# Kernel tuning notes

Hardware: AMD Instinct MI355X
Metric: run time of the kernel (lower is better)

The kernel has to match this reference:

```python
import jax, jax.numpy as jnp
import numpy as np

N = 100000   # nodes
E = 1600000  # edges


def setup_inputs() -> dict:
    key = jax.random.key(0)
    ks = jax.random.split(key, 9)
    return {
        "in_feat": jax.random.normal(ks[0], (N, 256), jnp.float32),
        "W": jax.random.normal(ks[1], (256, 128), jnp.float32) * 0.05,
        "attn_l": jax.random.normal(ks[2], (1, 128), jnp.float32) * 0.1,
        "attn_r": jax.random.normal(ks[3], (1, 128), jnp.float32) * 0.1,
        "bias": jax.random.normal(ks[4], (1, 128), jnp.float32) * 0.01,
        "fc_w": jax.random.normal(ks[5], (128, 2), jnp.float32) * 0.1,
        "fc_b": jax.random.normal(ks[6], (2,), jnp.float32) * 0.01,
        "src": jax.random.randint(ks[7], (E,), 0, N, jnp.int32),
        "dst": jax.random.randint(ks[8], (E,), 0, N, jnp.int32),
    }


def reference(in_feat, W, attn_l, attn_r, bias, fc_w, fc_b, src, dst):
    # GATConv, num_heads=1 (head dim kept implicit since it is squeezed anyway)
    h = in_feat @ W                              # [N, F] projected features
    el = jnp.sum(h * attn_l, axis=-1)            # [N] left attention logits
    er = jnp.sum(h * attn_r, axis=-1)            # [N] right attention logits
    e = jax.nn.leaky_relu(el[src] + er[dst], negative_slope=0.2)  # [E]
    # edge softmax segmented by destination node (numerically stable)
    m = jax.ops.segment_max(e, dst, num_segments=N)               # [N]
    ex = jnp.exp(e - m[dst])                                      # [E]
    s = jax.ops.segment_sum(ex, dst, num_segments=N)              # [N]
    alpha = ex / jnp.where(s == 0, 1.0, s)[dst]                   # [E]
    # attention-weighted aggregation of source features to destinations
    agg = jax.ops.segment_sum(alpha[:, None] * h[src], dst, num_segments=N)  # [N, F]
    agg = agg + bias                                              # GATConv bias
    # head: ReLU -> Linear -> sigmoid
    out = jax.nn.sigmoid(jax.nn.relu(agg) @ fc_w + fc_b)          # [N, C]
    return out
```

## Files before the change

### kernel.cpp

```cpp
#include <hip/hip_runtime.h>
#include <cstdint>
#include <cstddef>

#define N_NODES 100000
#define E_EDGES 1600000
#define F_IN 256
#define F_OUT 128
#define NBKT 391
#define OBCAP 5120

#define GLOBAL_AS __attribute__((address_space(1)))
#define LDS_AS    __attribute__((address_space(3)))

typedef __attribute__((ext_vector_type(8))) short  short8v;
typedef __attribute__((ext_vector_type(4))) float  float4v;

__device__ __forceinline__ unsigned short f2bf(float x) {
    union { float f; unsigned u; } v; v.f = x;
    unsigned r = v.u + 0x7fffu + ((v.u >> 16) & 1u);
    return (unsigned short)(r >> 16);
}

__device__ __forceinline__ unsigned cvt_pk_bf16(float lo, float hi) {
    unsigned r;
    asm("v_cvt_pk_bf16_f32 %0, %1, %2" : "=v"(r) : "v"(lo), "v"(hi));
    return r;
}

__global__ __launch_bounds__(256) void wcvt_kernel(const float* __restrict__ W,
                                                   unsigned short* __restrict__ Wt) {
    int t = blockIdx.x * 256 + threadIdx.x;
    if (t >= F_IN * F_OUT) return;
    int k = t >> 7, j = t & 127;
    Wt[j * F_IN + k] = f2bf(W[t]);
}

__global__ __launch_bounds__(256) void gemm_mfma(const float* __restrict__ A,
                                                 const unsigned short* __restrict__ Wt,
                                                 const float* __restrict__ attn_l,
                                                 const float* __restrict__ attn_r,
                                                 unsigned short* __restrict__ Hb,
                                                 float* __restrict__ el,
                                                 float* __restrict__ er) {
    __shared__ float          Afs[64 * 64];
    __shared__ unsigned short Bs[128 * 64];
    int tid  = threadIdx.x;
    int wave = tid >> 6, lane = tid & 63;
    int g = lane >> 4, c = lane & 15;
    int row0 = blockIdx.x * 64;
    float4v acc[8] = {};

    int a_r[4], a_k[4], a_w[4];
    #pragma unroll
    for (int i = 0; i < 4; ++i) {
        int W_ = i * 1024 + tid * 4;
        int r  = W_ >> 6;
        a_w[i] = W_;
        a_r[i] = min(row0 + r, N_NODES - 1);
        a_k[i] = (W_ & 63) ^ ((r & 15) << 2);
    }
    int b_j[4], b_k[4], b_u[4];
    #pragma unroll
    for (int i = 0; i < 4; ++i) {
        int U_ = i * 2048 + tid * 8;
        int j  = U_ >> 6;
        b_u[i] = U_;
        b_j[i] = j;
        b_k[i] = (U_ & 63) ^ ((j & 7) << 3);
    }

    for (int k0 = 0; k0 < F_IN; k0 += 64) {
        #pragma unroll
        for (int i = 0; i < 4; ++i) {
            __builtin_amdgcn_global_load_lds(
                (const GLOBAL_AS unsigned int*)(A + (size_t)a_r[i] * F_IN + k0 + a_k[i]),
                (LDS_AS unsigned int*)&Afs[a_w[i]], 16, 0, 0);
        }
        #pragma unroll
        for (int i = 0; i < 4; ++i) {
            __builtin_amdgcn_global_load_lds(
                (const GLOBAL_AS unsigned int*)(Wt + (size_t)b_j[i] * F_IN + k0 + b_k[i]),
                (LDS_AS unsigned int*)&Bs[b_u[i]], 16, 0, 0);
        }
        __syncthreads();
        int arow = wave * 16 + c;
        int aswz = (arow & 15) << 2;
        #pragma unroll
        for (int ks = 0; ks < 2; ++ks) {
            int woff = arow * 64 + ks * 32 + g * 8;
            float4 a0 = *reinterpret_cast<float4*>(&Afs[(woff)     ^ aswz]);
            float4 a1 = *reinterpret_cast<float4*>(&Afs[(woff + 4) ^ aswz]);
            unsigned u[4];
            u[0] = cvt_pk_bf16(a0.x, a0.y);
            u[1] = cvt_pk_bf16(a0.z, a0.w);
            u[2] = cvt_pk_bf16(a1.x, a1.y);
            u[3] = cvt_pk_bf16(a1.z, a1.w);
            short8v af = *reinterpret_cast<short8v*>(u);
            #pragma unroll
            for (int nt = 0; nt < 8; ++nt) {
                int j = nt * 16 + c;
                int boff = (j * 64 + ks * 32 + g * 8) ^ ((j & 7) << 3);
                short8v bf = *reinterpret_cast<short8v*>(&Bs[boff]);
                acc[nt] = __builtin_amdgcn_mfma_f32_16x16x32_bf16(af, bf, acc[nt], 0, 0, 0);
            }
        }
        __syncthreads();
    }

    float al[8], ar[8];
    #pragma unroll
    for (int nt = 0; nt < 8; ++nt) {
        al[nt] = attn_l[nt * 16 + c];
        ar[nt] = attn_r[nt * 16 + c];
    }
    #pragma unroll
    for (int r = 0; r < 4; ++r) {
        int grow = row0 + wave * 16 + g * 4 + r;
        float sl = 0.f, sr = 0.f;
        #pragma unroll
        for (int nt = 0; nt < 8; ++nt) {
            float h = acc[nt][r];
            sl += h * al[nt];
            sr += h * ar[nt];
        }
        if (grow < N_NODES) {
            #pragma unroll
            for (int nt = 0; nt < 8; ++nt)
                Hb[(size_t)grow * F_OUT + nt * 16 + c] = f2bf(acc[nt][r]);
        }
        #pragma unroll
        for (int off = 1; off < 16; off <<= 1) {
            sl += __shfl_xor(sl, off);
            sr += __shfl_xor(sr, off);
        }
        if (c == 0 && grow < N_NODES) { el[grow] = sl; er[grow] = sr; }
    }
}

__global__ __launch_bounds__(256) void k_hist1(const int* __restrict__ dst,
                                               int* __restrict__ bcnt) {
    __shared__ int h[NBKT];
    int t = threadIdx.x;
    for (int i = t; i < NBKT; i += 256) h[i] = 0;
    __syncthreads();
    int e0  = blockIdx.x * 4096;
    int end = min(e0 + 4096, E_EDGES);
    for (int i = e0 + t; i < end; i += 256) atomicAdd(&h[dst[i] >> 8], 1);
    __syncthreads();
    for (int i = t; i < NBKT; i += 256) if (h[i]) atomicAdd(&bcnt[i], h[i]);
}

__global__ __launch_bounds__(512) void k_scan(const int* __restrict__ bcnt,
                                              int* __restrict__ bbase,
                                              int* __restrict__ bcur) {
    __shared__ int s[512];
    int t = threadIdx.x;
    int d = (t < NBKT) ? bcnt[t] : 0;
    s[t] = d;
    __syncthreads();
    for (int off = 1; off < 512; off <<= 1) {
        int v = (t >= off) ? s[t - off] : 0;
        __syncthreads();
        s[t] += v;
        __syncthreads();
    }
    if (t < NBKT) { int ex = s[t] - d; bbase[t] = ex; bcur[t] = ex; }
    if (t == NBKT - 1) bbase[NBKT] = s[t];
}

__global__ __launch_bounds__(256) void k_scatter1(const int* __restrict__ src,
                                                  const int* __restrict__ dst,
                                                  int* __restrict__ bcur,
                                                  unsigned int* __restrict__ epack) {
    __shared__ int h[NBKT];
    int t = threadIdx.x;
    for (int i = t; i < NBKT; i += 256) h[i] = 0;
    __syncthreads();
    int e0  = blockIdx.x * 4096;
    int end = min(e0 + 4096, E_EDGES);
    #pragma unroll
    for (int j = 0; j < 16; ++j) {
        int i = e0 + j * 256 + t;
        if (i < end) atomicAdd(&h[dst[i] >> 8], 1);
    }
    __syncthreads();
    for (int i = t; i < NBKT; i += 256) {
        int c = h[i];
        h[i] = c ? atomicAdd(&bcur[i], c) : 0;
    }
    __syncthreads();
    #pragma unroll
    for (int j = 0; j < 16; ++j) {
        int i = e0 + j * 256 + t;
        if (i < end) {
            int dv = dst[i];
            int p = atomicAdd(&h[dv >> 8], 1);
            epack[p] = (unsigned)src[i] | ((unsigned)(dv & 255) << 17);
        }
    }
}

__global__ __launch_bounds__(256) void k_sort2(const unsigned int* __restrict__ epack,
                                               const int* __restrict__ bbase,
                                               int* __restrict__ esrc,
                                               int* __restrict__ rowptr,
                                               int* __restrict__ deg) {
    __shared__ int hist[256], cur[256], s[256];
    __shared__ int obuf[OBCAP];
    int b = blockIdx.x, t = threadIdx.x;
    int base = bbase[b], end = bbase[b + 1];
    int cnt  = end - base;
    hist[t] = 0;
    __syncthreads();
    for (int i = t; i < cnt; i += 256) atomicAdd(&hist[epack[base + i] >> 17], 1);
    __syncthreads();
    int d = hist[t];
    s[t] = d;
    __syncthreads();
    for (int off = 1; off < 256; off <<= 1) {
        int v = (t >= off) ? s[t - off] : 0;
        __syncthreads();
        s[t] += v;
        __syncthreads();
    }
    int excl = s[t] - d;
    int n = b * 256 + t;
    if (n < N_NODES) { deg[n] = d; rowptr[n] = base + excl; }
    cur[t] = excl;
    __syncthreads();
    for (int i = t; i < cnt; i += 256) {
        unsigned e = epack[base + i];
        int p = atomicAdd(&cur[e >> 17], 1);
        if (p < OBCAP) obuf[p] = (int)(e & 0x1FFFFu);
    }
    __syncthreads();
    for (int i = t; i < cnt; i += 256) esrc[base + i] = obuf[i];
}

__global__ __launch_bounds__(256) void agg_fused(const int* __restrict__ rowptr,
                                                 const int* __restrict__ deg,
                                                 const int* __restrict__ esrc,
                                                 const float* __restrict__ el,
                                                 const float* __restrict__ er,
                                                 const char* __restrict__ Hc,
                                                 const float* __restrict__ bias,
                                                 const float* __restrict__ fcw,
                                                 const float* __restrict__ fcb,
                                                 float* __restrict__ out) {
    __shared__ float2 exbuf[4][64];
    int tid   = threadIdx.x;
    int wslot = tid >> 6;
    int wid   = (blockIdx.x * 256 + tid) >> 6;
    int lane  = tid & 63;
    if (wid >= N_NODES) return;
    int grp = lane >> 4, fl = lane & 15;
    int start = rowptr[wid];
    int dg    = deg[wid];
    float ern = er[wid];
    float exsum = 0.f;
    float acc[8] = {};
    float2* eb = exbuf[wslot];
    unsigned flb = (unsigned)fl << 4;

    for (int base = 0; base < dg; base += 64) {
        int cnt = min(64, dg - base);
        unsigned rowb = 0;
        float ex = 0.f;
        if (lane < cnt) {
            int sid = esrc[start + base + lane];
            float tv = el[(unsigned)sid] + ern;
            tv = tv > 0.f ? tv : 0.2f * tv;
            ex = __expf(tv);
            rowb = (unsigned)sid << 8;
        }
        exsum += ex;
        eb[lane] = make_float2(ex, __uint_as_float(rowb));
        __builtin_amdgcn_wave_barrier();
        int nq = (cnt + 3) >> 2;
        #pragma unroll 2
        for (int q = 0; q < nq; ++q) {
            float2 p = eb[q * 4 + grp];
            float exq = p.x;
            uint4 v = *(const uint4*)(Hc + (__float_as_uint(p.y) + flb));
            acc[0] += exq * __uint_as_float(v.x << 16);
            acc[1] += exq * __uint_as_float(v.x & 0xffff0000u);
            acc[2] += exq * __uint_as_float(v.y << 16);
            acc[3] += exq * __uint_as_float(v.y & 0xffff0000u);
            acc[4] += exq * __uint_as_float(v.z << 16);
            acc[5] += exq * __uint_as_float(v.z & 0xffff0000u);
            acc[6] += exq * __uint_as_float(v.w << 16);
            acc[7] += exq * __uint_as_float(v.w & 0xffff0000u);
        }
        __builtin_amdgcn_wave_barrier();
    }

    #pragma unroll
    for (int j = 0; j < 8; ++j) {
        acc[j] += __shfl_xor(acc[j], 16);
        acc[j] += __shfl_xor(acc[j], 32);
    }
    float ssum = exsum;
    #pragma unroll
    for (int off = 32; off; off >>= 1) ssum += __shfl_xor(ssum, off);
    float scale = ssum > 0.f ? 1.f / ssum : 0.f;

    float4 b0 = ((const float4*)bias)[fl * 2];
    float4 b1 = ((const float4*)bias)[fl * 2 + 1];
    float d0 = 0.f, d1 = 0.f;
    #pragma unroll
    for (int j = 0; j < 8; ++j) {
        float bj = j < 4 ? (&b0.x)[j] : (&b1.x)[j - 4];
        float vv = fmaxf(acc[j] * scale + bj, 0.f);
        float2 wj = ((const float2*)fcw)[fl * 8 + j];
        d0 += vv * wj.x;
        d1 += vv * wj.y;
    }
    #pragma unroll
    for (int off = 1; off < 16; off <<= 1) {
        d0 += __shfl_xor(d0, off);
        d1 += __shfl_xor(d1, off);
    }
    if (lane == 0) {
        out[(size_t)wid * 2 + 0] = 1.f / (1.f + __expf(-(d0 + fcb[0])));
        out[(size_t)wid * 2 + 1] = 1.f / (1.f + __expf(-(d1 + fcb[1])));
    }
}

extern "C" void kernel_launch(void* const* d_in, const int* in_sizes, int n_in,
                              void* d_out, int out_size, void* d_ws, size_t ws_size,
                              hipStream_t stream) {
    const float* in_feat = (const float*)d_in[0];
    const float* W       = (const float*)d_in[1];
    const float* attn_l  = (const float*)d_in[2];
    const float* attn_r  = (const float*)d_in[3];
    const float* bias    = (const float*)d_in[4];
    const float* fc_w    = (const float*)d_in[5];
    const float* fc_b    = (const float*)d_in[6];
    const int*   src     = (const int*)d_in[7];
    const int*   dst     = (const int*)d_in[8];
    float* out = (float*)d_out;

    char* p = (char*)d_ws;
    unsigned short* HB = (unsigned short*)p; p += (size_t)N_NODES * F_OUT * sizeof(unsigned short);
    unsigned short* WT = (unsigned short*)p; p += (size_t)F_IN * F_OUT * sizeof(unsigned short);
    float* EL     = (float*)p; p += (size_t)N_NODES * sizeof(float);
    float* ER     = (float*)p; p += (size_t)N_NODES * sizeof(float);
    int*   DEG    = (int*)p;   p += (size_t)N_NODES * sizeof(int);
    int*   ROWPTR = (int*)p;   p += (size_t)N_NODES * sizeof(int);
    int*   BCNT   = (int*)p;   p += 512 * sizeof(int);
    int*   BBASE  = (int*)p;   p += 512 * sizeof(int);
    int*   BCUR   = (int*)p;   p += 512 * sizeof(int);
    unsigned int* EPACK = (unsigned int*)p; p += (size_t)E_EDGES * sizeof(unsigned int);
    int*   ESRC   = (int*)p;   p += (size_t)E_EDGES * sizeof(int);

    hipMemsetAsync(BCNT, 0, 512 * sizeof(int), stream);

    wcvt_kernel<<<(F_IN * F_OUT + 255) / 256, 256, 0, stream>>>(W, WT);
    gemm_mfma<<<(N_NODES + 63) / 64, 256, 0, stream>>>(in_feat, WT, attn_l, attn_r, HB, EL, ER);

    k_hist1   <<<NBKT, 256, 0, stream>>>(dst, BCNT);
    k_scan    <<<1, 512, 0, stream>>>(BCNT, BBASE, BCUR);
    k_scatter1<<<NBKT, 256, 0, stream>>>(src, dst, BCUR, EPACK);
    k_sort2   <<<NBKT, 256, 0, stream>>>(EPACK, BBASE, ESRC, ROWPTR, DEG);

    agg_fused<<<(N_NODES * 64 + 255) / 256, 256, 0, stream>>>(
        ROWPTR, DEG, ESRC, EL, ER, (const char*)HB, bias, fc_w, fc_b, out);
}
```

Measured before the change: 149.6 us.

## Merge weight conversion with histogram and GEMM with edge scatter launches

```diff
diff --git a/kernel.cpp b/kernel.cpp
--- a/kernel.cpp
+++ b/kernel.cpp
@@ -8,6 +8,8 @@
 #define F_OUT 128
 #define NBKT 391
 #define OBCAP 5120
+#define GEMM_NB 1563
+#define WCVT_NB 128
 
 #define GLOBAL_AS __attribute__((address_space(1)))
 #define LDS_AS    __attribute__((address_space(3)))
@@ -27,24 +29,92 @@
     return r;
 }
 
-__global__ __launch_bounds__(256) void wcvt_kernel(const float* __restrict__ W,
-                                                   unsigned short* __restrict__ Wt) {
-    int t = blockIdx.x * 256 + threadIdx.x;
-    if (t >= F_IN * F_OUT) return;
-    int k = t >> 7, j = t & 127;
-    Wt[j * F_IN + k] = f2bf(W[t]);
-}
-
-__global__ __launch_bounds__(256) void gemm_mfma(const float* __restrict__ A,
-                                                 const unsigned short* __restrict__ Wt,
-                                                 const float* __restrict__ attn_l,
-                                                 const float* __restrict__ attn_r,
-                                                 unsigned short* __restrict__ Hb,
-                                                 float* __restrict__ el,
-                                                 float* __restrict__ er) {
-    __shared__ float          Afs[64 * 64];
-    __shared__ unsigned short Bs[128 * 64];
-    int tid  = threadIdx.x;
+__global__ __launch_bounds__(256) void wcvt_hist(const float* __restrict__ W,
+                                                 unsigned short* __restrict__ Wt,
+                                                 const int* __restrict__ dst,
+                                                 int* __restrict__ bcnt) {
+    __shared__ int h[NBKT];
+    int t = threadIdx.x;
+    if (blockIdx.x < WCVT_NB) {
+        int i = blockIdx.x * 256 + t;
+        int k = i >> 7, j = i & 127;
+        Wt[j * F_IN + k] = f2bf(W[i]);
+        return;
+    }
+    int b = blockIdx.x - WCVT_NB;
+    for (int i = t; i < NBKT; i += 256) h[i] = 0;
+    __syncthreads();
+    int e0  = b * 4096;
+    int end = min(e0 + 4096, E_EDGES);
+    for (int i = e0 + t; i < end; i += 256) atomicAdd(&h[dst[i] >> 8], 1);
+    __syncthreads();
+    for (int i = t; i < NBKT; i += 256) if (h[i]) atomicAdd(&bcnt[i], h[i]);
+}
+
+__global__ __launch_bounds__(512) void k_scan(const int* __restrict__ bcnt,
+                                              int* __restrict__ bbase,
+                                              int* __restrict__ bcur) {
+    __shared__ int s[512];
+    int t = threadIdx.x;
+    int d = (t < NBKT) ? bcnt[t] : 0;
+    s[t] = d;
+    __syncthreads();
+    for (int off = 1; off < 512; off <<= 1) {
+        int v = (t >= off) ? s[t - off] : 0;
+        __syncthreads();
+        s[t] += v;
+        __syncthreads();
+    }
+    if (t < NBKT) { int ex = s[t] - d; bbase[t] = ex; bcur[t] = ex; }
+    if (t == NBKT - 1) bbase[NBKT] = s[t];
+}
+
+__global__ __launch_bounds__(256) void gemm_scatter(const float* __restrict__ A,
+                                                    const unsigned short* __restrict__ Wt,
+                                                    const float* __restrict__ attn_l,
+                                                    const float* __restrict__ attn_r,
+                                                    unsigned short* __restrict__ Hb,
+                                                    float* __restrict__ el,
+                                                    float* __restrict__ er,
+                                                    const int* __restrict__ src,
+                                                    const int* __restrict__ dst,
+                                                    int* __restrict__ bcur,
+                                                    unsigned int* __restrict__ epack) {
+    __shared__ char smem[32 * 1024];
+    int tid = threadIdx.x;
+
+    if (blockIdx.x >= GEMM_NB) {
+        int* h = (int*)smem;
+        int b = blockIdx.x - GEMM_NB;
+        for (int i = tid; i < NBKT; i += 256) h[i] = 0;
+        __syncthreads();
+        int e0  = b * 4096;
+        int end = min(e0 + 4096, E_EDGES);
+        #pragma unroll
+        for (int j = 0; j < 16; ++j) {
+            int i = e0 + j * 256 + tid;
+            if (i < end) atomicAdd(&h[dst[i] >> 8], 1);
+        }
+        __syncthreads();
+        for (int i = tid; i < NBKT; i += 256) {
+            int c = h[i];
+            h[i] = c ? atomicAdd(&bcur[i], c) : 0;
+        }
+        __syncthreads();
+        #pragma unroll
+        for (int j = 0; j < 16; ++j) {
+            int i = e0 + j * 256 + tid;
+            if (i < end) {
+                int dv = dst[i];
+                int p = atomicAdd(&h[dv >> 8], 1);
+                epack[p] = (unsigned)src[i] | ((unsigned)(dv & 255) << 17);
+            }
+        }
+        return;
+    }
+
+    float*          Afs = (float*)smem;
+    unsigned short* Bs  = (unsigned short*)(smem + 16 * 1024);
     int wave = tid >> 6, lane = tid & 63;
     int g = lane >> 4, c = lane & 15;
     int row0 = blockIdx.x * 64;
@@ -137,69 +207,6 @@
     }
 }
 
-__global__ __launch_bounds__(256) void k_hist1(const int* __restrict__ dst,
-                                               int* __restrict__ bcnt) {
-    __shared__ int h[NBKT];
-    int t = threadIdx.x;
-    for (int i = t; i < NBKT; i += 256) h[i] = 0;
-    __syncthreads();
-    int e0  = blockIdx.x * 4096;
-    int end = min(e0 + 4096, E_EDGES);
-    for (int i = e0 + t; i < end; i += 256) atomicAdd(&h[dst[i] >> 8], 1);
-    __syncthreads();
-    for (int i = t; i < NBKT; i += 256) if (h[i]) atomicAdd(&bcnt[i], h[i]);
-}
-
-__global__ __launch_bounds__(512) void k_scan(const int* __restrict__ bcnt,
-                                              int* __restrict__ bbase,
-                                              int* __restrict__ bcur) {
-    __shared__ int s[512];
-    int t = threadIdx.x;
-    int d = (t < NBKT) ? bcnt[t] : 0;
-    s[t] = d;
-    __syncthreads();
-    for (int off = 1; off < 512; off <<= 1) {
-        int v = (t >= off) ? s[t - off] : 0;
-        __syncthreads();
-        s[t] += v;
-        __syncthreads();
-    }
-    if (t < NBKT) { int ex = s[t] - d; bbase[t] = ex; bcur[t] = ex; }
-    if (t == NBKT - 1) bbase[NBKT] = s[t];
-}
-
-__global__ __launch_bounds__(256) void k_scatter1(const int* __restrict__ src,
-                                                  const int* __restrict__ dst,
-                                                  int* __restrict__ bcur,
-                                                  unsigned int* __restrict__ epack) {
-    __shared__ int h[NBKT];
-    int t = threadIdx.x;
-    for (int i = t; i < NBKT; i += 256) h[i] = 0;
-    __syncthreads();
-    int e0  = blockIdx.x * 4096;
-    int end = min(e0 + 4096, E_EDGES);
-    #pragma unroll
-    for (int j = 0; j < 16; ++j) {
-        int i = e0 + j * 256 + t;
-        if (i < end) atomicAdd(&h[dst[i] >> 8], 1);
-    }
-    __syncthreads();
-    for (int i = t; i < NBKT; i += 256) {
-        int c = h[i];
-        h[i] = c ? atomicAdd(&bcur[i], c) : 0;
-    }
-    __syncthreads();
-    #pragma unroll
-    for (int j = 0; j < 16; ++j) {
-        int i = e0 + j * 256 + t;
-        if (i < end) {
-            int dv = dst[i];
-            int p = atomicAdd(&h[dv >> 8], 1);
-            epack[p] = (unsigned)src[i] | ((unsigned)(dv & 255) << 17);
-        }
-    }
-}
-
 __global__ __launch_bounds__(256) void k_sort2(const unsigned int* __restrict__ epack,
                                                const int* __restrict__ bbase,
                                                int* __restrict__ esrc,
@@ -247,11 +254,9 @@
                                                  const float* __restrict__ fcw,
                                                  const float* __restrict__ fcb,
                                                  float* __restrict__ out) {
-    __shared__ float2 exbuf[4][64];
-    int tid   = threadIdx.x;
-    int wslot = tid >> 6;
-    int wid   = (blockIdx.x * 256 + tid) >> 6;
-    int lane  = tid & 63;
+    int tid  = threadIdx.x;
+    int wid  = (blockIdx.x * 256 + tid) >> 6;
+    int lane = tid & 63;
     if (wid >= N_NODES) return;
     int grp = lane >> 4, fl = lane & 15;
     int start = rowptr[wid];
@@ -259,49 +264,34 @@
     float ern = er[wid];
     float exsum = 0.f;
     float acc[8] = {};
-    float2* eb = exbuf[wslot];
     unsigned flb = (unsigned)fl << 4;
 
-    for (int base = 0; base < dg; base += 64) {
-        int cnt = min(64, dg - base);
-        unsigned rowb = 0;
-        float ex = 0.f;
-        if (lane < cnt) {
-            int sid = esrc[start + base + lane];
-            float tv = el[(unsigned)sid] + ern;
-            tv = tv > 0.f ? tv : 0.2f * tv;
-            ex = __expf(tv);
-            rowb = (unsigned)sid << 8;
-        }
+    #pragma unroll 2
+    for (int q = grp; q < dg; q += 4) {
+        int sid = esrc[start + q];
+        float tv = el[(unsigned)sid] + ern;
+        tv = tv > 0.f ? tv : 0.2f * tv;
+        float ex = __expf(tv);
         exsum += ex;
-        eb[lane] = make_float2(ex, __uint_as_float(rowb));
-        __builtin_amdgcn_wave_barrier();
-        int nq = (cnt + 3) >> 2;
-        #pragma unroll 2
-        for (int q = 0; q < nq; ++q) {
-            float2 p = eb[q * 4 + grp];
-            float exq = p.x;
-            uint4 v = *(const uint4*)(Hc + (__float_as_uint(p.y) + flb));
-            acc[0] += exq * __uint_as_float(v.x << 16);
-            acc[1] += exq * __uint_as_float(v.x & 0xffff0000u);
-            acc[2] += exq * __uint_as_float(v.y << 16);
-            acc[3] += exq * __uint_as_float(v.y & 0xffff0000u);
-            acc[4] += exq * __uint_as_float(v.z << 16);
-            acc[5] += exq * __uint_as_float(v.z & 0xffff0000u);
-            acc[6] += exq * __uint_as_float(v.w << 16);
-            acc[7] += exq * __uint_as_float(v.w & 0xffff0000u);
-        }
-        __builtin_amdgcn_wave_barrier();
-    }
-
+        uint4 v = *(const uint4*)(Hc + (((unsigned)sid << 8) + flb));
+        acc[0] += ex * __uint_as_float(v.x << 16);
+        acc[1] += ex * __uint_as_float(v.x & 0xffff0000u);
+        acc[2] += ex * __uint_as_float(v.y << 16);
+        acc[3] += ex * __uint_as_float(v.y & 0xffff0000u);
+        acc[4] += ex * __uint_as_float(v.z << 16);
+        acc[5] += ex * __uint_as_float(v.z & 0xffff0000u);
+        acc[6] += ex * __uint_as_float(v.w << 16);
+        acc[7] += ex * __uint_as_float(v.w & 0xffff0000u);
+    }
+
+    float ssum = exsum;
+    ssum += __shfl_xor(ssum, 16);
+    ssum += __shfl_xor(ssum, 32);
     #pragma unroll
     for (int j = 0; j < 8; ++j) {
         acc[j] += __shfl_xor(acc[j], 16);
         acc[j] += __shfl_xor(acc[j], 32);
     }
-    float ssum = exsum;
-    #pragma unroll
-    for (int off = 32; off; off >>= 1) ssum += __shfl_xor(ssum, off);
     float scale = ssum > 0.f ? 1.f / ssum : 0.f;
 
     float4 b0 = ((const float4*)bias)[fl * 2];
@@ -355,13 +345,11 @@
 
     hipMemsetAsync(BCNT, 0, 512 * sizeof(int), stream);
 
-    wcvt_kernel<<<(F_IN * F_OUT + 255) / 256, 256, 0, stream>>>(W, WT);
-    gemm_mfma<<<(N_NODES + 63) / 64, 256, 0, stream>>>(in_feat, WT, attn_l, attn_r, HB, EL, ER);
-
-    k_hist1   <<<NBKT, 256, 0, stream>>>(dst, BCNT);
-    k_scan    <<<1, 512, 0, stream>>>(BCNT, BBASE, BCUR);
-    k_scatter1<<<NBKT, 256, 0, stream>>>(src, dst, BCUR, EPACK);
-    k_sort2   <<<NBKT, 256, 0, stream>>>(EPACK, BBASE, ESRC, ROWPTR, DEG);
+    wcvt_hist<<<WCVT_NB + NBKT, 256, 0, stream>>>(W, WT, dst, BCNT);
+    k_scan   <<<1, 512, 0, stream>>>(BCNT, BBASE, BCUR);
+    gemm_scatter<<<GEMM_NB + NBKT, 256, 0, stream>>>(
+        in_feat, WT, attn_l, attn_r, HB, EL, ER, src, dst, BCUR, EPACK);
+    k_sort2  <<<NBKT, 256, 0, stream>>>(EPACK, BBASE, ESRC, ROWPTR, DEG);
 
     agg_fused<<<(N_NODES * 64 + 255) / 256, 256, 0, stream>>>(
         ROWPTR, DEG, ESRC, EL, ER, (const char*)HB, bias, fc_w, fc_b, out);
```

After: 150.2 us. About the same (+0.4%).
